# Kernel tuning notes

Hardware: AMD Instinct MI355X
Metric: run time of the kernel (lower is better)

## Reference

```python
import jax, jax.numpy as jnp
import numpy as np

SEQ_LEN = 256
SPIKE_STEPS = 7
BATCH = 128
IN_DIM = 96
HIDDEN = 512
OUT_DIM = 2
NLAYERS = 3
ALPHA = 2.0  # atan surrogate alpha = 2 * grad_slope


@jax.custom_vjp
def spike(x):
    # Heaviside fire with snntorch ATan surrogate gradient.
    return (x > 0).astype(x.dtype)


def _spike_fwd(x):
    return (x > 0).astype(x.dtype), x


def _spike_bwd(x, g):
    return (g * (ALPHA / 2.0) / (1.0 + (jnp.pi / 2.0 * ALPHA * x) ** 2),)


spike.defvjp(_spike_fwd, _spike_bwd)


def setup_inputs() -> dict:
    key = jax.random.key(0)
    ks = jax.random.split(key, 5)
    x = jax.random.normal(ks[0], (SEQ_LEN, BATCH, IN_DIM), dtype=jnp.float32)
    def w(k, shape, fan_in):
        return jax.random.normal(k, shape, dtype=jnp.float32) / np.float32(np.sqrt(fan_in))
    W0 = w(ks[1], (HIDDEN, IN_DIM), IN_DIM)
    W1 = w(ks[2], (HIDDEN, HIDDEN), HIDDEN)
    W2 = w(ks[3], (HIDDEN, HIDDEN), HIDDEN)
    Wout = w(ks[4], (OUT_DIM, HIDDEN), HIDDEN)
    betas = jnp.full((NLAYERS,), 0.95, dtype=jnp.float32)  # learnable beta per LIF layer
    thrs = jnp.ones((NLAYERS,), dtype=jnp.float32)          # learnable threshold per LIF layer
    return dict(x=x, W0=W0, W1=W1, W2=W2, Wout=Wout, betas=betas, thrs=thrs)


def reference(x, W0, W1, W2, Wout, betas, thrs):
    """Seq2SeqSNN forward (eval mode: dropout is identity).

    Membrane / integrator state is reset only once at the start (i == 0 path
    of the torch forward), so the whole seq_len * spike_steps loop is a single
    recurrence of length T = SEQ_LEN * SPIKE_STEPS.
    LIF layer (snntorch Leaky, reset_mechanism='zero'):
        reset = stop_grad(heaviside(mem_prev - thr))
        mem   = (beta * mem_prev + cur) * (1 - reset)
        spk   = spike(mem - thr)
    Output layer (Integrator, reset 'none'): mem_out += Wout @ z; the decoded
    prediction per sequence step is the mean of mem_out over spike_steps.
    """
    Ws = (W0, W1, W2)
    x_rep = jnp.repeat(x, SPIKE_STEPS, axis=0)  # [T, B, F], same input for each inner spike step

    mems0 = tuple(jnp.zeros((BATCH, HIDDEN), dtype=x.dtype) for _ in range(NLAYERS))
    mem_out0 = jnp.zeros((BATCH, OUT_DIM), dtype=x.dtype)

    def step(carry, xt):
        mems, mem_out = carry
        z = xt
        new_mems = []
        for j in range(NLAYERS):
            cur = z @ Ws[j].T                                   # [B, H]
            reset = jax.lax.stop_gradient(spike(mems[j] - thrs[j]))
            mem = (betas[j] * mems[j] + cur) * (1.0 - reset)
            z = spike(mem - thrs[j])                            # binary spikes
            new_mems.append(mem)
        mem_out = mem_out + z @ Wout.T                           # integrator, no reset
        return (tuple(new_mems), mem_out), mem_out

    _, mem_out_seq = jax.lax.scan(step, (mems0, mem_out0), x_rep)  # [T, B, 2]
    # decoder='mean' over the spike_steps axis of each sequence step
    preds = mem_out_seq.reshape(SEQ_LEN, SPIKE_STEPS, BATCH, OUT_DIM).mean(axis=1)
    return preds  # [SEQ_LEN, BATCH, OUT_DIM]
```

## Files before the change

kernel.cpp:

```cpp
#include <hip/hip_runtime.h>

#define SEQ_LEN 256
#define SPIKE_STEPS 7
#define BATCH 128
#define IN_DIM 96
#define HIDDEN 512
#define OUT_DIM 2

#define W0T_OFF 0
#define W1T_OFF (IN_DIM * HIDDEN)
#define W2T_OFF (W1T_OFF + HIDDEN * HIDDEN)
#define CTR_BYTE_OFF ((size_t)(W2T_OFF + HIDDEN * HIDDEN) * sizeof(float))
#define ZBUF_BYTE_OFF (CTR_BYTE_OFF + 1024)

typedef float f32x4 __attribute__((ext_vector_type(4)));
typedef float f32x2 __attribute__((ext_vector_type(2)));

__global__ void transpose_kernel(const float* __restrict__ in, float* __restrict__ out,
                                 int rows, int cols) {
    int idx = blockIdx.x * blockDim.x + threadIdx.x;
    if (idx < rows * cols) {
        int r = idx / cols, c = idx - r * cols;
        out[c * rows + r] = in[idx];
    }
}

__device__ __forceinline__ void pkfma(f32x2& acc, float w, f32x2 m) {
    const f32x2 wv = {w, w};
    acc = __builtin_elementwise_fma(wv, m, acc);
}

__device__ __forceinline__ void union_sum7_2(const float* __restrict__ W,
                                             const int* __restrict__ act,
                                             const float (* __restrict__ fmp)[8],
                                             int npad, int tid,
                                             f32x2* __restrict__ accA,
                                             f32x2* __restrict__ accB) {
    if (npad <= 0) return;
    const float* WtA = W + tid;
    const float* WtB = W + tid + 256;
    int rows[16];
    float wcA[16], wcB[16];
    {
        const int4* av = reinterpret_cast<const int4*>(act);
        int4 a0 = av[0], a1 = av[1], a2 = av[2], a3 = av[3];
        rows[0]=a0.x; rows[1]=a0.y; rows[2]=a0.z; rows[3]=a0.w;
        rows[4]=a1.x; rows[5]=a1.y; rows[6]=a1.z; rows[7]=a1.w;
        rows[8]=a2.x; rows[9]=a2.y; rows[10]=a2.z; rows[11]=a2.w;
        rows[12]=a3.x; rows[13]=a3.y; rows[14]=a3.z; rows[15]=a3.w;
    }
    #pragma unroll
    for (int k = 0; k < 16; ++k) {
        wcA[k] = WtA[rows[k] * HIDDEN];
        wcB[k] = WtB[rows[k] * HIDDEN];
    }

    for (int n = 16; n < npad; n += 16) {
        int nrows[16];
        float wnA[16], wnB[16];
        {
            const int4* av = reinterpret_cast<const int4*>(act + n);
            int4 a0 = av[0], a1 = av[1], a2 = av[2], a3 = av[3];
            nrows[0]=a0.x; nrows[1]=a0.y; nrows[2]=a0.z; nrows[3]=a0.w;
            nrows[4]=a1.x; nrows[5]=a1.y; nrows[6]=a1.z; nrows[7]=a1.w;
            nrows[8]=a2.x; nrows[9]=a2.y; nrows[10]=a2.z; nrows[11]=a2.w;
            nrows[12]=a3.x; nrows[13]=a3.y; nrows[14]=a3.z; nrows[15]=a3.w;
        }
        #pragma unroll
        for (int k = 0; k < 16; ++k) {
            wnA[k] = WtA[nrows[k] * HIDDEN];
            wnB[k] = WtB[nrows[k] * HIDDEN];
        }

        const int base = n - 16;
        #pragma unroll
        for (int k = 0; k < 16; ++k) {
            f32x4 fa = *reinterpret_cast<const f32x4*>(&fmp[base + k][0]);
            f32x4 fb = *reinterpret_cast<const f32x4*>(&fmp[base + k][4]);
            f32x2 m01 = __builtin_shufflevector(fa, fa, 0, 1);
            f32x2 m23 = __builtin_shufflevector(fa, fa, 2, 3);
            f32x2 m45 = __builtin_shufflevector(fb, fb, 0, 1);
            f32x2 m67 = __builtin_shufflevector(fb, fb, 2, 3);
            pkfma(accA[0], wcA[k], m01);
            pkfma(accA[1], wcA[k], m23);
            pkfma(accA[2], wcA[k], m45);
            pkfma(accA[3], wcA[k], m67);
            pkfma(accB[0], wcB[k], m01);
            pkfma(accB[1], wcB[k], m23);
            pkfma(accB[2], wcB[k], m45);
            pkfma(accB[3], wcB[k], m67);
        }
        #pragma unroll
        for (int k = 0; k < 16; ++k) { wcA[k] = wnA[k]; wcB[k] = wnB[k]; }
    }
    const int base = npad - 16;
    #pragma unroll
    for (int k = 0; k < 16; ++k) {
        f32x4 fa = *reinterpret_cast<const f32x4*>(&fmp[base + k][0]);
        f32x4 fb = *reinterpret_cast<const f32x4*>(&fmp[base + k][4]);
        f32x2 m01 = __builtin_shufflevector(fa, fa, 0, 1);
        f32x2 m23 = __builtin_shufflevector(fa, fa, 2, 3);
        f32x2 m45 = __builtin_shufflevector(fb, fb, 0, 1);
        f32x2 m67 = __builtin_shufflevector(fb, fb, 2, 3);
        pkfma(accA[0], wcA[k], m01);
        pkfma(accA[1], wcA[k], m23);
        pkfma(accA[2], wcA[k], m45);
        pkfma(accA[3], wcA[k], m67);
        pkfma(accB[0], wcB[k], m01);
        pkfma(accB[1], wcB[k], m23);
        pkfma(accB[2], wcB[k], m45);
        pkfma(accB[3], wcB[k], m67);
    }
}

__device__ __forceinline__ int build_union(const unsigned long long (*zm7)[8],
                                           int* act, float (*fmp)[8],
                                           int wid, int lane, int tid, int m7) {
    unsigned long long um[8];
    #pragma unroll
    for (int q = 0; q < 8; ++q) {
        unsigned long long u = zm7[0][q];
        #pragma unroll
        for (int s = 1; s < SPIKE_STEPS; ++s) u |= zm7[s][q];
        um[q] = u;
    }
    int pre = 0, total = 0;
    #pragma unroll
    for (int q = 0; q < 8; ++q) {
        int p = __popcll(um[q]);
        total += p;
        if (q < wid) pre += p;
    }
    if (m7 != 0) {
        int rank = pre + __popcll(um[wid] & ((1ull << lane) - 1ull));
        act[rank] = tid;
        f32x4 v0, v4;
        #pragma unroll
        for (int s = 0; s < 4; ++s) v0[s] = ((m7 >> s) & 1) ? 1.0f : 0.0f;
        #pragma unroll
        for (int s = 0; s < 3; ++s) v4[s] = ((m7 >> (4 + s)) & 1) ? 1.0f : 0.0f;
        v4[3] = 0.f;
        *reinterpret_cast<f32x4*>(&fmp[rank][0]) = v0;
        *reinterpret_cast<f32x4*>(&fmp[rank][4]) = v4;
    }
    int npad = (total + 15) & ~15;
    if (tid < npad - total) {
        act[total + tid] = 0;
        const f32x4 z = {0.f, 0.f, 0.f, 0.f};
        *reinterpret_cast<f32x4*>(&fmp[total + tid][0]) = z;
        *reinterpret_cast<f32x4*>(&fmp[total + tid][4]) = z;
    }
    return npad;
}

__launch_bounds__(512, 1)
__global__ void snn_pipe_kernel(const float* __restrict__ x,
                                const float* __restrict__ Wout,
                                const float* __restrict__ betas,
                                const float* __restrict__ thrs,
                                const float* __restrict__ W0T,
                                const float* __restrict__ W1T,
                                const float* __restrict__ W2T,
                                unsigned long long* __restrict__ zbuf,
                                int* __restrict__ ctr,
                                float* __restrict__ out)
{
    const int b    = blockIdx.x >> 1;
    const int role = blockIdx.x & 1;
    const int tid  = threadIdx.x;
    const int lane = tid & 63;
    const int wid  = tid >> 6;
    const bool mv  = (tid < 256);

    __shared__ float xs[2][IN_DIM];
    __shared__ unsigned long long zm7[SPIKE_STEPS][8];
    __shared__ int act[HIDDEN];
    __shared__ __align__(16) float fmp[HIDDEN][8];
    __shared__ float red[8];

    if (role == 0) {
        const float beta0 = betas[0], beta1 = betas[1];
        const float thr0  = thrs[0],  thr1  = thrs[1];
        float mem0 = 0.f;
        float mem1A = 0.f, mem1B = 0.f;
        unsigned long long* zb = zbuf + (size_t)b * SEQ_LEN * 56;

        if (tid < IN_DIM) xs[0][tid] = x[(0 * BATCH + b) * IN_DIM + tid];
        __syncthreads();

        for (int i = 0; i < SEQ_LEN; ++i) {
            const int cur = i & 1;

            float cur0 = 0.f;
            #pragma unroll 8
            for (int k = 0; k < IN_DIM; ++k)
                cur0 = __fmaf_rn(xs[cur][k], W0T[k * HIDDEN + tid], cur0);

            if (i + 1 < SEQ_LEN && tid < IN_DIM)
                xs[cur ^ 1][tid] = x[((i + 1) * BATCH + b) * IN_DIM + tid];

            int m7 = 0;
            #pragma unroll
            for (int s = 0; s < SPIKE_STEPS; ++s) {
                bool reset0 = (mem0 - thr0) > 0.f;
                mem0 = reset0 ? 0.f : __fadd_rn(__fmul_rn(beta0, mem0), cur0);
                bool z0 = (mem0 - thr0) > 0.f;
                m7 |= (int)z0 << s;
                unsigned long long bal = __ballot(z0);
                if (lane == 0) zm7[s][wid] = bal;
            }
            __syncthreads();

            int npad = build_union(zm7, act, fmp, wid, lane, tid, m7);
            __syncthreads();

            if (mv) {
                f32x2 accA[4] = {{0.f,0.f},{0.f,0.f},{0.f,0.f},{0.f,0.f}};
                f32x2 accB[4] = {{0.f,0.f},{0.f,0.f},{0.f,0.f},{0.f,0.f}};
                union_sum7_2(W1T, act, fmp, npad, tid, accA, accB);
                const float accsA[SPIKE_STEPS] =
                    {accA[0].x, accA[0].y, accA[1].x, accA[1].y, accA[2].x, accA[2].y, accA[3].x};
                const float accsB[SPIKE_STEPS] =
                    {accB[0].x, accB[0].y, accB[1].x, accB[1].y, accB[2].x, accB[2].y, accB[3].x};

                #pragma unroll
                for (int s = 0; s < SPIKE_STEPS; ++s) {
                    bool r1A = (mem1A - thr1) > 0.f;
                    mem1A = r1A ? 0.f : __fadd_rn(__fmul_rn(beta1, mem1A), accsA[s]);
                    bool z1A = (mem1A - thr1) > 0.f;
                    bool r1B = (mem1B - thr1) > 0.f;
                    mem1B = r1B ? 0.f : __fadd_rn(__fmul_rn(beta1, mem1B), accsB[s]);
                    bool z1B = (mem1B - thr1) > 0.f;
                    unsigned long long balA = __ballot(z1A);
                    unsigned long long balB = __ballot(z1B);
                    if (lane == 0) {
                        __hip_atomic_store(&zb[(size_t)i * 56 + s * 8 + wid], balA,
                                           __ATOMIC_RELAXED, __HIP_MEMORY_SCOPE_AGENT);
                        __hip_atomic_store(&zb[(size_t)i * 56 + s * 8 + 4 + wid], balB,
                                           __ATOMIC_RELAXED, __HIP_MEMORY_SCOPE_AGENT);
                    }
                }
            }
            __syncthreads();
            if (tid == 0)
                __hip_atomic_store(&ctr[b], i + 1,
                                   __ATOMIC_RELAXED, __HIP_MEMORY_SCOPE_AGENT);
        }
    } else {
        const float beta2 = betas[2];
        const float thr2  = thrs[2];
        const int cB = (tid & 255) + 256;
        const float wo0A = Wout[tid & 255];
        const float wo0B = Wout[cB];
        const float wo1A = Wout[HIDDEN + (tid & 255)];
        const float wo1B = Wout[HIDDEN + cB];
        float mem2A = 0.f, mem2B = 0.f;
        float a0s = 0.f, a1s = 0.f;
        const unsigned long long* zb = zbuf + (size_t)b * SEQ_LEN * 56;

        for (int i = 0; i < SEQ_LEN; ++i) {
            if (tid < 56) {
                while (__hip_atomic_load(&ctr[b], __ATOMIC_RELAXED,
                                         __HIP_MEMORY_SCOPE_AGENT) < i + 1)
                    __builtin_amdgcn_s_sleep(1);
                ((unsigned long long*)zm7)[tid] =
                    __hip_atomic_load(&zb[(size_t)i * 56 + tid],
                                      __ATOMIC_RELAXED, __HIP_MEMORY_SCOPE_AGENT);
            }
            __syncthreads();

            int m7 = 0;
            #pragma unroll
            for (int s = 0; s < SPIKE_STEPS; ++s)
                m7 |= (int)((zm7[s][wid] >> lane) & 1ull) << s;

            int npad = build_union(zm7, act, fmp, wid, lane, tid, m7);
            __syncthreads();

            if (mv) {
                f32x2 accA[4] = {{0.f,0.f},{0.f,0.f},{0.f,0.f},{0.f,0.f}};
                f32x2 accB[4] = {{0.f,0.f},{0.f,0.f},{0.f,0.f},{0.f,0.f}};
                union_sum7_2(W2T, act, fmp, npad, tid, accA, accB);
                const float accsA[SPIKE_STEPS] =
                    {accA[0].x, accA[0].y, accA[1].x, accA[1].y, accA[2].x, accA[2].y, accA[3].x};
                const float accsB[SPIKE_STEPS] =
                    {accB[0].x, accB[0].y, accB[1].x, accB[1].y, accB[2].x, accB[2].y, accB[3].x};

                float w0 = 0.f, w1 = 0.f;
                #pragma unroll
                for (int s = 0; s < SPIKE_STEPS; ++s) {
                    bool r2A = (mem2A - thr2) > 0.f;
                    mem2A = r2A ? 0.f : __fadd_rn(__fmul_rn(beta2, mem2A), accsA[s]);
                    bool z2A = (mem2A - thr2) > 0.f;
                    bool r2B = (mem2B - thr2) > 0.f;
                    mem2B = r2B ? 0.f : __fadd_rn(__fmul_rn(beta2, mem2B), accsB[s]);
                    bool z2B = (mem2B - thr2) > 0.f;
                    a0s += z2A ? wo0A : 0.f;
                    a0s += z2B ? wo0B : 0.f;
                    a1s += z2A ? wo1A : 0.f;
                    a1s += z2B ? wo1B : 0.f;
                    w0 += a0s;
                    w1 += a1s;
                }

                float r0 = w0, r1 = w1;
                #pragma unroll
                for (int off = 32; off > 0; off >>= 1) {
                    r0 += __shfl_down(r0, off);
                    r1 += __shfl_down(r1, off);
                }
                if (lane == 0) { red[wid * 2] = r0; red[wid * 2 + 1] = r1; }
            }
            __syncthreads();
            if (tid == 0) {
                float s0 = 0.f, s1 = 0.f;
                #pragma unroll
                for (int q = 0; q < 4; ++q) { s0 += red[q * 2]; s1 += red[q * 2 + 1]; }
                out[(i * BATCH + b) * OUT_DIM + 0] = s0 / 7.0f;
                out[(i * BATCH + b) * OUT_DIM + 1] = s1 / 7.0f;
            }
        }
    }
}

extern "C" void kernel_launch(void* const* d_in, const int* in_sizes, int n_in,
                              void* d_out, int out_size, void* d_ws, size_t ws_size,
                              hipStream_t stream) {
    const float* x     = (const float*)d_in[0];
    const float* W0    = (const float*)d_in[1];
    const float* W1    = (const float*)d_in[2];
    const float* W2    = (const float*)d_in[3];
    const float* Wout  = (const float*)d_in[4];
    const float* betas = (const float*)d_in[5];
    const float* thrs  = (const float*)d_in[6];
    float* out = (float*)d_out;

    float* ws  = (float*)d_ws;
    float* W0T = ws + W0T_OFF;
    float* W1T = ws + W1T_OFF;
    float* W2T = ws + W2T_OFF;
    int* ctr = (int*)((char*)d_ws + CTR_BYTE_OFF);
    unsigned long long* zbuf = (unsigned long long*)((char*)d_ws + ZBUF_BYTE_OFF);

    {
        int n = HIDDEN * IN_DIM;
        transpose_kernel<<<(n + 255) / 256, 256, 0, stream>>>(W0, W0T, HIDDEN, IN_DIM);
    }
    {
        int n = HIDDEN * HIDDEN;
        transpose_kernel<<<(n + 255) / 256, 256, 0, stream>>>(W1, W1T, HIDDEN, HIDDEN);
        transpose_kernel<<<(n + 255) / 256, 256, 0, stream>>>(W2, W2T, HIDDEN, HIDDEN);
    }

    hipMemsetAsync((char*)d_ws + CTR_BYTE_OFF, 0, 1024, stream);

    snn_pipe_kernel<<<2 * BATCH, HIDDEN, 0, stream>>>(
        x, Wout, betas, thrs, W0T, W1T, W2T, zbuf, ctr, out);
}
```

Baseline: 2.927 ms.

## Fuse two-block layer pipeline into one block per batch element

Replaces the producer/consumer pair of blocks per batch element, which passed layer-1 spikes through global memory with a spin-wait counter, with a single block that runs all three layers in sequence and exchanges spikes through shared memory. This drops the global stores, the polling and the memset, and halves the grid to 128 blocks. The cost is that layer 1 and layer 2 no longer overlap across blocks, so each time step's critical path now contains both sparse matvecs serially.

Result: slower. 4.794 ms (+63.8%).

```diff
diff --git a/kernel.cpp b/kernel.cpp
--- a/kernel.cpp
+++ b/kernel.cpp
@@ -10,8 +10,6 @@
 #define W0T_OFF 0
 #define W1T_OFF (IN_DIM * HIDDEN)
 #define W2T_OFF (W1T_OFF + HIDDEN * HIDDEN)
-#define CTR_BYTE_OFF ((size_t)(W2T_OFF + HIDDEN * HIDDEN) * sizeof(float))
-#define ZBUF_BYTE_OFF (CTR_BYTE_OFF + 1024)
 
 typedef float f32x4 __attribute__((ext_vector_type(4)));
 typedef float f32x2 __attribute__((ext_vector_type(2)));
@@ -154,171 +152,146 @@
 }
 
 __launch_bounds__(512, 1)
-__global__ void snn_pipe_kernel(const float* __restrict__ x,
-                                const float* __restrict__ Wout,
-                                const float* __restrict__ betas,
-                                const float* __restrict__ thrs,
-                                const float* __restrict__ W0T,
-                                const float* __restrict__ W1T,
-                                const float* __restrict__ W2T,
-                                unsigned long long* __restrict__ zbuf,
-                                int* __restrict__ ctr,
-                                float* __restrict__ out)
+__global__ void snn_fused_kernel(const float* __restrict__ x,
+                                 const float* __restrict__ Wout,
+                                 const float* __restrict__ betas,
+                                 const float* __restrict__ thrs,
+                                 const float* __restrict__ W0T,
+                                 const float* __restrict__ W1T,
+                                 const float* __restrict__ W2T,
+                                 float* __restrict__ out)
 {
-    const int b    = blockIdx.x >> 1;
-    const int role = blockIdx.x & 1;
+    const int b    = blockIdx.x;
     const int tid  = threadIdx.x;
     const int lane = tid & 63;
     const int wid  = tid >> 6;
     const bool mv  = (tid < 256);
 
-    __shared__ float xs[2][IN_DIM];
+    __shared__ __align__(16) float xs[2][IN_DIM];
     __shared__ unsigned long long zm7[SPIKE_STEPS][8];
     __shared__ int act[HIDDEN];
     __shared__ __align__(16) float fmp[HIDDEN][8];
     __shared__ float red[8];
 
-    if (role == 0) {
-        const float beta0 = betas[0], beta1 = betas[1];
-        const float thr0  = thrs[0],  thr1  = thrs[1];
-        float mem0 = 0.f;
-        float mem1A = 0.f, mem1B = 0.f;
-        unsigned long long* zb = zbuf + (size_t)b * SEQ_LEN * 56;
-
-        if (tid < IN_DIM) xs[0][tid] = x[(0 * BATCH + b) * IN_DIM + tid];
-        __syncthreads();
-
-        for (int i = 0; i < SEQ_LEN; ++i) {
-            const int cur = i & 1;
-
-            float cur0 = 0.f;
-            #pragma unroll 8
-            for (int k = 0; k < IN_DIM; ++k)
-                cur0 = __fmaf_rn(xs[cur][k], W0T[k * HIDDEN + tid], cur0);
-
-            if (i + 1 < SEQ_LEN && tid < IN_DIM)
-                xs[cur ^ 1][tid] = x[((i + 1) * BATCH + b) * IN_DIM + tid];
-
-            int m7 = 0;
+    const float beta0 = betas[0], beta1 = betas[1], beta2 = betas[2];
+    const float thr0  = thrs[0],  thr1  = thrs[1],  thr2  = thrs[2];
+
+    float mem0 = 0.f;
+    float mem1A = 0.f, mem1B = 0.f;
+    float mem2A = 0.f, mem2B = 0.f;
+    float a0s = 0.f, a1s = 0.f;
+    const int cA = tid & 255;
+    const int cB = cA + 256;
+    const float wo0A = Wout[cA];
+    const float wo0B = Wout[cB];
+    const float wo1A = Wout[HIDDEN + cA];
+    const float wo1B = Wout[HIDDEN + cB];
+
+    if (tid < IN_DIM) xs[0][tid] = x[(0 * BATCH + b) * IN_DIM + tid];
+    __syncthreads();
+
+    for (int i = 0; i < SEQ_LEN; ++i) {
+        const int cur = i & 1;
+
+        float cur0 = 0.f;
+        #pragma unroll 8
+        for (int k = 0; k < IN_DIM; ++k)
+            cur0 = __fmaf_rn(xs[cur][k], W0T[k * HIDDEN + tid], cur0);
+
+        if (i + 1 < SEQ_LEN && tid < IN_DIM)
+            xs[cur ^ 1][tid] = x[((i + 1) * BATCH + b) * IN_DIM + tid];
+
+        int m7 = 0;
+        #pragma unroll
+        for (int s = 0; s < SPIKE_STEPS; ++s) {
+            bool reset0 = (mem0 - thr0) > 0.f;
+            mem0 = reset0 ? 0.f : __fadd_rn(__fmul_rn(beta0, mem0), cur0);
+            bool z0 = (mem0 - thr0) > 0.f;
+            m7 |= (int)z0 << s;
+            unsigned long long bal = __ballot(z0);
+            if (lane == 0) zm7[s][wid] = bal;
+        }
+        __syncthreads();
+
+        int npad = build_union(zm7, act, fmp, wid, lane, tid, m7);
+        __syncthreads();
+
+        if (mv) {
+            f32x2 accA[4] = {{0.f,0.f},{0.f,0.f},{0.f,0.f},{0.f,0.f}};
+            f32x2 accB[4] = {{0.f,0.f},{0.f,0.f},{0.f,0.f},{0.f,0.f}};
+            union_sum7_2(W1T, act, fmp, npad, tid, accA, accB);
+            const float accsA[SPIKE_STEPS] =
+                {accA[0].x, accA[0].y, accA[1].x, accA[1].y, accA[2].x, accA[2].y, accA[3].x};
+            const float accsB[SPIKE_STEPS] =
+                {accB[0].x, accB[0].y, accB[1].x, accB[1].y, accB[2].x, accB[2].y, accB[3].x};
+
             #pragma unroll
             for (int s = 0; s < SPIKE_STEPS; ++s) {
-                bool reset0 = (mem0 - thr0) > 0.f;
-                mem0 = reset0 ? 0.f : __fadd_rn(__fmul_rn(beta0, mem0), cur0);
-                bool z0 = (mem0 - thr0) > 0.f;
-                m7 |= (int)z0 << s;
-                unsigned long long bal = __ballot(z0);
-                if (lane == 0) zm7[s][wid] = bal;
-            }
-            __syncthreads();
-
-            int npad = build_union(zm7, act, fmp, wid, lane, tid, m7);
-            __syncthreads();
-
-            if (mv) {
-                f32x2 accA[4] = {{0.f,0.f},{0.f,0.f},{0.f,0.f},{0.f,0.f}};
-                f32x2 accB[4] = {{0.f,0.f},{0.f,0.f},{0.f,0.f},{0.f,0.f}};
-                union_sum7_2(W1T, act, fmp, npad, tid, accA, accB);
-                const float accsA[SPIKE_STEPS] =
-                    {accA[0].x, accA[0].y, accA[1].x, accA[1].y, accA[2].x, accA[2].y, accA[3].x};
-                const float accsB[SPIKE_STEPS] =
-                    {accB[0].x, accB[0].y, accB[1].x, accB[1].y, accB[2].x, accB[2].y, accB[3].x};
-
-                #pragma unroll
-                for (int s = 0; s < SPIKE_STEPS; ++s) {
-                    bool r1A = (mem1A - thr1) > 0.f;
-                    mem1A = r1A ? 0.f : __fadd_rn(__fmul_rn(beta1, mem1A), accsA[s]);
-                    bool z1A = (mem1A - thr1) > 0.f;
-                    bool r1B = (mem1B - thr1) > 0.f;
-                    mem1B = r1B ? 0.f : __fadd_rn(__fmul_rn(beta1, mem1B), accsB[s]);
-                    bool z1B = (mem1B - thr1) > 0.f;
-                    unsigned long long balA = __ballot(z1A);
-                    unsigned long long balB = __ballot(z1B);
-                    if (lane == 0) {
-                        __hip_atomic_store(&zb[(size_t)i * 56 + s * 8 + wid], balA,
-                                           __ATOMIC_RELAXED, __HIP_MEMORY_SCOPE_AGENT);
-                        __hip_atomic_store(&zb[(size_t)i * 56 + s * 8 + 4 + wid], balB,
-                                           __ATOMIC_RELAXED, __HIP_MEMORY_SCOPE_AGENT);
-                    }
+                bool r1A = (mem1A - thr1) > 0.f;
+                mem1A = r1A ? 0.f : __fadd_rn(__fmul_rn(beta1, mem1A), accsA[s]);
+                bool z1A = (mem1A - thr1) > 0.f;
+                bool r1B = (mem1B - thr1) > 0.f;
+                mem1B = r1B ? 0.f : __fadd_rn(__fmul_rn(beta1, mem1B), accsB[s]);
+                bool z1B = (mem1B - thr1) > 0.f;
+                unsigned long long balA = __ballot(z1A);
+                unsigned long long balB = __ballot(z1B);
+                if (lane == 0) {
+                    zm7[s][wid] = balA;
+                    zm7[s][4 + wid] = balB;
                 }
             }
-            __syncthreads();
-            if (tid == 0)
-                __hip_atomic_store(&ctr[b], i + 1,
-                                   __ATOMIC_RELAXED, __HIP_MEMORY_SCOPE_AGENT);
-        }
-    } else {
-        const float beta2 = betas[2];
-        const float thr2  = thrs[2];
-        const int cB = (tid & 255) + 256;
-        const float wo0A = Wout[tid & 255];
-        const float wo0B = Wout[cB];
-        const float wo1A = Wout[HIDDEN + (tid & 255)];
-        const float wo1B = Wout[HIDDEN + cB];
-        float mem2A = 0.f, mem2B = 0.f;
-        float a0s = 0.f, a1s = 0.f;
-        const unsigned long long* zb = zbuf + (size_t)b * SEQ_LEN * 56;
-
-        for (int i = 0; i < SEQ_LEN; ++i) {
-            if (tid < 56) {
-                while (__hip_atomic_load(&ctr[b], __ATOMIC_RELAXED,
-                                         __HIP_MEMORY_SCOPE_AGENT) < i + 1)
-                    __builtin_amdgcn_s_sleep(1);
-                ((unsigned long long*)zm7)[tid] =
-                    __hip_atomic_load(&zb[(size_t)i * 56 + tid],
-                                      __ATOMIC_RELAXED, __HIP_MEMORY_SCOPE_AGENT);
+        }
+        __syncthreads();
+
+        int m7b = 0;
+        #pragma unroll
+        for (int s = 0; s < SPIKE_STEPS; ++s)
+            m7b |= (int)((zm7[s][wid] >> lane) & 1ull) << s;
+
+        npad = build_union(zm7, act, fmp, wid, lane, tid, m7b);
+        __syncthreads();
+
+        if (mv) {
+            f32x2 accA[4] = {{0.f,0.f},{0.f,0.f},{0.f,0.f},{0.f,0.f}};
+            f32x2 accB[4] = {{0.f,0.f},{0.f,0.f},{0.f,0.f},{0.f,0.f}};
+            union_sum7_2(W2T, act, fmp, npad, tid, accA, accB);
+            const float accsA[SPIKE_STEPS] =
+                {accA[0].x, accA[0].y, accA[1].x, accA[1].y, accA[2].x, accA[2].y, accA[3].x};
+            const float accsB[SPIKE_STEPS] =
+                {accB[0].x, accB[0].y, accB[1].x, accB[1].y, accB[2].x, accB[2].y, accB[3].x};
+
+            float w0 = 0.f, w1 = 0.f;
+            #pragma unroll
+            for (int s = 0; s < SPIKE_STEPS; ++s) {
+                bool r2A = (mem2A - thr2) > 0.f;
+                mem2A = r2A ? 0.f : __fadd_rn(__fmul_rn(beta2, mem2A), accsA[s]);
+                bool z2A = (mem2A - thr2) > 0.f;
+                bool r2B = (mem2B - thr2) > 0.f;
+                mem2B = r2B ? 0.f : __fadd_rn(__fmul_rn(beta2, mem2B), accsB[s]);
+                bool z2B = (mem2B - thr2) > 0.f;
+                a0s += z2A ? wo0A : 0.f;
+                a0s += z2B ? wo0B : 0.f;
+                a1s += z2A ? wo1A : 0.f;
+                a1s += z2B ? wo1B : 0.f;
+                w0 += a0s;
+                w1 += a1s;
             }
-            __syncthreads();
-
-            int m7 = 0;
+
+            float r0 = w0, r1 = w1;
             #pragma unroll
-            for (int s = 0; s < SPIKE_STEPS; ++s)
-                m7 |= (int)((zm7[s][wid] >> lane) & 1ull) << s;
-
-            int npad = build_union(zm7, act, fmp, wid, lane, tid, m7);
-            __syncthreads();
-
-            if (mv) {
-                f32x2 accA[4] = {{0.f,0.f},{0.f,0.f},{0.f,0.f},{0.f,0.f}};
-                f32x2 accB[4] = {{0.f,0.f},{0.f,0.f},{0.f,0.f},{0.f,0.f}};
-                union_sum7_2(W2T, act, fmp, npad, tid, accA, accB);
-                const float accsA[SPIKE_STEPS] =
-                    {accA[0].x, accA[0].y, accA[1].x, accA[1].y, accA[2].x, accA[2].y, accA[3].x};
-                const float accsB[SPIKE_STEPS] =
-                    {accB[0].x, accB[0].y, accB[1].x, accB[1].y, accB[2].x, accB[2].y, accB[3].x};
-
-                float w0 = 0.f, w1 = 0.f;
-                #pragma unroll
-                for (int s = 0; s < SPIKE_STEPS; ++s) {
-                    bool r2A = (mem2A - thr2) > 0.f;
-                    mem2A = r2A ? 0.f : __fadd_rn(__fmul_rn(beta2, mem2A), accsA[s]);
-                    bool z2A = (mem2A - thr2) > 0.f;
-                    bool r2B = (mem2B - thr2) > 0.f;
-                    mem2B = r2B ? 0.f : __fadd_rn(__fmul_rn(beta2, mem2B), accsB[s]);
-                    bool z2B = (mem2B - thr2) > 0.f;
-                    a0s += z2A ? wo0A : 0.f;
-                    a0s += z2B ? wo0B : 0.f;
-                    a1s += z2A ? wo1A : 0.f;
-                    a1s += z2B ? wo1B : 0.f;
-                    w0 += a0s;
-                    w1 += a1s;
-                }
-
-                float r0 = w0, r1 = w1;
-                #pragma unroll
-                for (int off = 32; off > 0; off >>= 1) {
-                    r0 += __shfl_down(r0, off);
-                    r1 += __shfl_down(r1, off);
-                }
-                if (lane == 0) { red[wid * 2] = r0; red[wid * 2 + 1] = r1; }
+            for (int off = 32; off > 0; off >>= 1) {
+                r0 += __shfl_down(r0, off);
+                r1 += __shfl_down(r1, off);
             }
-            __syncthreads();
-            if (tid == 0) {
-                float s0 = 0.f, s1 = 0.f;
-                #pragma unroll
-                for (int q = 0; q < 4; ++q) { s0 += red[q * 2]; s1 += red[q * 2 + 1]; }
-                out[(i * BATCH + b) * OUT_DIM + 0] = s0 / 7.0f;
-                out[(i * BATCH + b) * OUT_DIM + 1] = s1 / 7.0f;
-            }
+            if (lane == 0) { red[wid * 2] = r0; red[wid * 2 + 1] = r1; }
+        }
+        __syncthreads();
+        if (tid == 0) {
+            float s0 = 0.f, s1 = 0.f;
+            #pragma unroll
+            for (int q = 0; q < 4; ++q) { s0 += red[q * 2]; s1 += red[q * 2 + 1]; }
+            out[(i * BATCH + b) * OUT_DIM + 0] = s0 / 7.0f;
+            out[(i * BATCH + b) * OUT_DIM + 1] = s1 / 7.0f;
         }
     }
 }
@@ -339,8 +312,6 @@
     float* W0T = ws + W0T_OFF;
     float* W1T = ws + W1T_OFF;
     float* W2T = ws + W2T_OFF;
-    int* ctr = (int*)((char*)d_ws + CTR_BYTE_OFF);
-    unsigned long long* zbuf = (unsigned long long*)((char*)d_ws + ZBUF_BYTE_OFF);
 
     {
         int n = HIDDEN * IN_DIM;
@@ -352,8 +323,6 @@
         transpose_kernel<<<(n + 255) / 256, 256, 0, stream>>>(W2, W2T, HIDDEN, HIDDEN);
     }
 
-    hipMemsetAsync((char*)d_ws + CTR_BYTE_OFF, 0, 1024, stream);
-
-    snn_pipe_kernel<<<2 * BATCH, HIDDEN, 0, stream>>>(
-        x, Wout, betas, thrs, W0T, W1T, W2T, zbuf, ctr, out);
-}
+    snn_fused_kernel<<<BATCH, HIDDEN, 0, stream>>>(
+        x, Wout, betas, thrs, W0T, W1T, W2T, out);
+}
```
